# Optimization experiments

Hardware: AMD Instinct MI355X
Metric: run time of the kernel (lower is better)

Reference implementation:

```python
import jax, jax.numpy as jnp
import numpy as np

K_NEIGHBORS = 5
LEAKY_SLOPE = 0.2
NEG_INF = -1e9


def create_knn(x, k):
    # x: [B, N, D] -> binary adjacency [B, N, N], adj[b,i,j]=1 if j is among
    # the k nearest neighbors of i (squared euclidean distance).
    sq = jnp.sum(x * x, axis=-1)                      # [B, N]
    # d2[b,i,j] = |xi|^2 + |xj|^2 - 2 xi.xj
    d2 = sq[:, :, None] + sq[:, None, :] - 2.0 * jnp.einsum('bid,bjd->bij', x, x)
    _, idx = jax.lax.top_k(-d2, k)                    # [B, N, k] nearest (incl. self)
    B, N, _ = x.shape
    b_idx = jnp.arange(B)[:, None, None]
    i_idx = jnp.arange(N)[None, :, None]
    adj = jnp.zeros((B, N, N), dtype=x.dtype).at[b_idx, i_idx, idx].set(1.0)
    return adj


def gat_layer(x, adj, W, a_src, a_dst):
    # Single-head GAT over dense kNN adjacency.
    h = jnp.einsum('bnd,df->bnf', x, W)               # [B, N, F]
    e_src = jnp.einsum('bnf,f->bn', h, a_src)         # [B, N]
    e_dst = jnp.einsum('bnf,f->bn', h, a_dst)         # [B, N]
    e = e_src[:, :, None] + e_dst[:, None, :]         # [B, N, N]
    e = jax.nn.leaky_relu(e, negative_slope=LEAKY_SLOPE)
    e = jnp.where(adj > 0, e, NEG_INF)
    alpha = jax.nn.softmax(e, axis=-1)                # [B, N, N]
    out = jnp.einsum('bij,bjf->bif', alpha, h)        # [B, N, F]
    return jax.nn.elu(out)


def setup_inputs() -> dict:
    key = jax.random.key(0)
    k1, k2, k3, k4 = jax.random.split(key, 4)
    B, N, D = 256, 196, 2048
    F = D // 4
    return {
        'resnet_features': jax.random.normal(k1, (B, N, D), dtype=jnp.float32),
        'W': jax.random.normal(k2, (D, F), dtype=jnp.float32) * (1.0 / np.sqrt(D)),
        'a_src': jax.random.normal(k3, (F,), dtype=jnp.float32) * (1.0 / np.sqrt(F)),
        'a_dst': jax.random.normal(k4, (F,), dtype=jnp.float32) * (1.0 / np.sqrt(F)),
    }


def reference(resnet_features, W, a_src, a_dst):
    adj = create_knn(resnet_features, K_NEIGHBORS)
    return gat_layer(resnet_features, adj, W, a_src, a_dst)
```

## Files before the change

### kernel.cpp

```cpp
#include <hip/hip_runtime.h>

#define B_  256
#define N_  196
#define D_  2048
#define F_  512
#define ROWS (B_*N_)
#define CAND 8
#define PROWS 208
#define PELEMS (PROWS*32)

typedef _Float16 f16x8 __attribute__((ext_vector_type(8)));
typedef _Float16 f16x4 __attribute__((ext_vector_type(4)));
typedef float    f32x4 __attribute__((ext_vector_type(4)));

static __device__ __forceinline__ float wave_reduce_sum(float v) {
#pragma unroll
  for (int off = 32; off > 0; off >>= 1) v += __shfl_xor(v, off);
  return v;
}

static __device__ __forceinline__ double wave_reduce_sum_d(double v) {
#pragma unroll
  for (int off = 32; off > 0; off >>= 1) v += __shfl_xor(v, off);
  return v;
}

static __device__ __forceinline__ float np_chain16(const float* __restrict__ x, int h) {
  int base = (h >> 3) * 128 + (h & 7);
  float t0 = x[base];
  float r = __fmul_rn(t0, t0);
#pragma unroll
  for (int i = 1; i < 16; ++i) {
    float t = x[base + 8 * i];
    r = __fadd_rn(r, __fmul_rn(t, t));
  }
  return r;
}
static __device__ __forceinline__ float np_sq_row(const float* __restrict__ x, int lane) {
  float ra = np_chain16(x, lane);
  float rb = np_chain16(x, lane + 64);
#pragma unroll
  for (int off = 1; off <= 4; off <<= 1) {
    ra = __fadd_rn(ra, __shfl_xor(ra, off));
    rb = __fadd_rn(rb, __shfl_xor(rb, off));
  }
  float lf[16];
#pragma unroll
  for (int L = 0; L < 8; ++L) { lf[L] = __shfl(ra, L * 8); lf[8 + L] = __shfl(rb, L * 8); }
  float b8[8];
#pragma unroll
  for (int t = 0; t < 8; ++t) b8[t] = __fadd_rn(lf[2 * t], lf[2 * t + 1]);
  float c4[4];
#pragma unroll
  for (int t = 0; t < 4; ++t) c4[t] = __fadd_rn(b8[2 * t], b8[2 * t + 1]);
  return __fadd_rn(__fadd_rn(c4[0], c4[1]), __fadd_rn(c4[2], c4[3]));
}

__global__ __launch_bounds__(256) void wtrans_kernel(const float* __restrict__ W,
                                                     _Float16* __restrict__ Wt2) {
  __shared__ float T[64][68];
  int k0 = blockIdx.x * 64;
  int f0 = blockIdx.y * 64;
  int tid = threadIdx.x;
  int c = tid & 63;
  int r4 = tid >> 6;
#pragma unroll
  for (int p = 0; p < 16; ++p) {
    int r = p * 4 + r4;
    T[r][c] = W[(size_t)(k0 + r) * F_ + f0 + c];
  }
  __syncthreads();
#pragma unroll
  for (int p = 0; p < 16; ++p) {
    int fr = p * 4 + r4;
    int kg = k0 + c;
    Wt2[(size_t)(kg >> 5) * F_ * 32 + (size_t)(f0 + fr) * 32 + (kg & 31)] = (_Float16)T[c][fr];
  }
}

__global__ __launch_bounds__(256, 3) void h_gemm(const float* __restrict__ X,
                                                 const _Float16* __restrict__ Wt2,
                                                 float* __restrict__ H) {
  __shared__ _Float16 Al[2][64][40];
  const int mBase = blockIdx.y * 64;
  const int nBase = blockIdx.x * 256;
  const int tid  = threadIdx.x;
  const int lane = tid & 63;
  const int wave = tid >> 6;
  const int fr_row = lane & 15;
  const int fr_k   = (lane >> 4) * 8;
  const int ar = tid >> 2;
  const int ak = (tid & 3) * 8;
  f32x4 acc[4][4] = {};

  const _Float16* Bb = Wt2 + (size_t)(nBase + wave * 64 + fr_row) * 32 + fr_k;
  const size_t PSTRIDE = (size_t)F_ * 32;

  f16x8 bf[4];
#pragma unroll
  for (int n = 0; n < 4; ++n) bf[n] = *(const f16x8*)&Bb[(size_t)n * 512];

  {
    float4 a0 = *(const float4*)&X[(size_t)(mBase + ar) * D_ + ak];
    float4 a1 = *(const float4*)&X[(size_t)(mBase + ar) * D_ + ak + 4];
    f16x8 ah = { (_Float16)a0.x, (_Float16)a0.y, (_Float16)a0.z, (_Float16)a0.w,
                 (_Float16)a1.x, (_Float16)a1.y, (_Float16)a1.z, (_Float16)a1.w };
    *(f16x8*)&Al[0][ar][ak] = ah;
  }
  __syncthreads();

  for (int t = 0; t < 64; ++t) {
    const int cur = t & 1;
    float4 na0, na1; f16x8 nb[4];
    if (t < 63) {
      const int k0 = (t + 1) * 32;
      na0 = *(const float4*)&X[(size_t)(mBase + ar) * D_ + k0 + ak];
      na1 = *(const float4*)&X[(size_t)(mBase + ar) * D_ + k0 + ak + 4];
      const _Float16* bp = Bb + (size_t)(t + 1) * PSTRIDE;
#pragma unroll
      for (int n = 0; n < 4; ++n) nb[n] = *(const f16x8*)&bp[(size_t)n * 512];
    }
    f16x8 af[4];
#pragma unroll
    for (int m = 0; m < 4; ++m) af[m] = *(const f16x8*)&Al[cur][m * 16 + fr_row][fr_k];
#pragma unroll
    for (int m = 0; m < 4; ++m)
#pragma unroll
      for (int n = 0; n < 4; ++n)
        acc[m][n] = __builtin_amdgcn_mfma_f32_16x16x32_f16(af[m], bf[n], acc[m][n], 0, 0, 0);
    if (t < 63) {
      f16x8 ah = { (_Float16)na0.x, (_Float16)na0.y, (_Float16)na0.z, (_Float16)na0.w,
                   (_Float16)na1.x, (_Float16)na1.y, (_Float16)na1.z, (_Float16)na1.w };
      *(f16x8*)&Al[cur ^ 1][ar][ak] = ah;
#pragma unroll
      for (int n = 0; n < 4; ++n) bf[n] = nb[n];
    }
    __syncthreads();
  }

  const int orow0 = mBase + (lane >> 4) * 4;
#pragma unroll
  for (int m = 0; m < 4; ++m) {
#pragma unroll
    for (int n = 0; n < 4; ++n) {
      int col = nBase + wave * 64 + n * 16 + (lane & 15);
#pragma unroll
      for (int i = 0; i < 4; ++i)
        H[(size_t)(orow0 + m * 16 + i) * F_ + col] = acc[m][n][i];
    }
  }
}

__global__ __launch_bounds__(256, 3) void h_gemm_pan(const float* __restrict__ X,
                                                     const _Float16* __restrict__ Wt2,
                                                     float* __restrict__ H,
                                                     _Float16* __restrict__ Xh,
                                                     float* __restrict__ sqg) {
  __shared__ _Float16 Al[2][64][40];
  __shared__ float sqs[64][4];
  const int mBase = blockIdx.y * 64;
  const int nBase = blockIdx.x * 256;
  const bool emit = (blockIdx.x == 0);
  const int tid  = threadIdx.x;
  const int lane = tid & 63;
  const int wave = tid >> 6;
  const int fr_row = lane & 15;
  const int fr_k   = (lane >> 4) * 8;
  const int ar = tid >> 2;
  const int ak = (tid & 3) * 8;
  f32x4 acc[4][4] = {};
  float sqp = 0.f;

  const int grow = mBase + ar;
  const int bb = grow / N_;
  const int rl = grow - bb * N_;
  _Float16* pRow = Xh + (size_t)bb * 64 * PELEMS + (size_t)rl * 32 + ak;

  const _Float16* Bb = Wt2 + (size_t)(nBase + wave * 64 + fr_row) * 32 + fr_k;
  const size_t PSTRIDE = (size_t)F_ * 32;

  f16x8 bf[4];
#pragma unroll
  for (int n = 0; n < 4; ++n) bf[n] = *(const f16x8*)&Bb[(size_t)n * 512];

  {
    float4 a0 = *(const float4*)&X[(size_t)(mBase + ar) * D_ + ak];
    float4 a1 = *(const float4*)&X[(size_t)(mBase + ar) * D_ + ak + 4];
    f16x8 ah = { (_Float16)a0.x, (_Float16)a0.y, (_Float16)a0.z, (_Float16)a0.w,
                 (_Float16)a1.x, (_Float16)a1.y, (_Float16)a1.z, (_Float16)a1.w };
    *(f16x8*)&Al[0][ar][ak] = ah;
    if (emit) {
      sqp += a0.x*a0.x + a0.y*a0.y + a0.z*a0.z + a0.w*a0.w
           + a1.x*a1.x + a1.y*a1.y + a1.z*a1.z + a1.w*a1.w;
      *(f16x8*)pRow = ah;
    }
  }
  __syncthreads();

  for (int t = 0; t < 64; ++t) {
    const int cur = t & 1;
    float4 na0, na1; f16x8 nb[4];
    if (t < 63) {
      const int k0 = (t + 1) * 32;
      na0 = *(const float4*)&X[(size_t)(mBase + ar) * D_ + k0 + ak];
      na1 = *(const float4*)&X[(size_t)(mBase + ar) * D_ + k0 + ak + 4];
      const _Float16* bp = Bb + (size_t)(t + 1) * PSTRIDE;
#pragma unroll
      for (int n = 0; n < 4; ++n) nb[n] = *(const f16x8*)&bp[(size_t)n * 512];
    }
    f16x8 af[4];
#pragma unroll
    for (int m = 0; m < 4; ++m) af[m] = *(const f16x8*)&Al[cur][m * 16 + fr_row][fr_k];
#pragma unroll
    for (int m = 0; m < 4; ++m)
#pragma unroll
      for (int n = 0; n < 4; ++n)
        acc[m][n] = __builtin_amdgcn_mfma_f32_16x16x32_f16(af[m], bf[n], acc[m][n], 0, 0, 0);
    if (t < 63) {
      f16x8 ah = { (_Float16)na0.x, (_Float16)na0.y, (_Float16)na0.z, (_Float16)na0.w,
                   (_Float16)na1.x, (_Float16)na1.y, (_Float16)na1.z, (_Float16)na1.w };
      *(f16x8*)&Al[cur ^ 1][ar][ak] = ah;
      if (emit) {
        sqp += na0.x*na0.x + na0.y*na0.y + na0.z*na0.z + na0.w*na0.w
             + na1.x*na1.x + na1.y*na1.y + na1.z*na1.z + na1.w*na1.w;
        *(f16x8*)(pRow + (size_t)(t + 1) * PELEMS) = ah;
      }
#pragma unroll
      for (int n = 0; n < 4; ++n) bf[n] = nb[n];
    }
    __syncthreads();
  }

  if (emit) sqs[ar][tid & 3] = sqp;
  __syncthreads();
  if (emit && tid < 64)
    sqg[mBase + tid] = sqs[tid][0] + sqs[tid][1] + sqs[tid][2] + sqs[tid][3];

  const int orow0 = mBase + (lane >> 4) * 4;
#pragma unroll
  for (int m = 0; m < 4; ++m) {
#pragma unroll
    for (int n = 0; n < 4; ++n) {
      int col = nBase + wave * 64 + n * 16 + (lane & 15);
#pragma unroll
      for (int i = 0; i < 4; ++i)
        H[(size_t)(orow0 + m * 16 + i) * F_ + col] = acc[m][n][i];
    }
  }
}

__global__ __launch_bounds__(256) void e_kernel(const float* __restrict__ H,
                                                const float* __restrict__ as,
                                                const float* __restrict__ ad,
                                                float* __restrict__ es,
                                                float* __restrict__ ed) {
  int row  = blockIdx.x * 4 + (threadIdx.x >> 6);
  int lane = threadIdx.x & 63;
  const float* h = H + (size_t)row * F_;
  float s = 0.f, d = 0.f;
#pragma unroll
  for (int p = 0; p < 2; ++p) {
    int col = p * 256 + lane * 4;
    float4 hv = *(const float4*)&h[col];
    float4 av = *(const float4*)&as[col];
    float4 dv = *(const float4*)&ad[col];
    s += hv.x * av.x + hv.y * av.y + hv.z * av.z + hv.w * av.w;
    d += hv.x * dv.x + hv.y * dv.y + hv.z * dv.z + hv.w * dv.w;
  }
  s = wave_reduce_sum(s);
  d = wave_reduce_sum(d);
  if (lane == 0) { es[row] = s; ed[row] = d; }
}

__global__ __launch_bounds__(256, 3) void knn_screen(const float* __restrict__ X,
                                                     int* __restrict__ cand8,
                                                     float* __restrict__ gapw) {
  __shared__ _Float16 T[2][256][40];
  __shared__ float sqA[256];

  const int bi  = blockIdx.x;
  const int xcd = bi & 7;
  const int kk  = bi >> 3;
  const int b   = ((kk >> 2) << 3) | xcd;
  const int i0  = (kk & 3) * 64;

  const int tid  = threadIdx.x;
  const int lane = tid & 63;
  const int wave = tid >> 6;
  const float* Xb = X + (size_t)b * N_ * D_;
  const int fr_row = lane & 15;
  const int fr_k   = (lane >> 4) * 8;
  const int srow = tid >> 3;
  const int skk  = (tid & 7) * 4;

  f32x4 acc[13] = {};
  float sqp[8] = {};

  {
    float4 v[8];
#pragma unroll
    for (int p = 0; p < 8; ++p) {
      int r = p * 32 + srow;
      v[p] = make_float4(0.f, 0.f, 0.f, 0.f);
      if (r < N_) v[p] = *(const float4*)&Xb[(size_t)r * D_ + skk];
    }
#pragma unroll
    for (int p = 0; p < 8; ++p) {
      int r = p * 32 + srow;
      sqp[p] += v[p].x * v[p].x + v[p].y * v[p].y + v[p].z * v[p].z + v[p].w * v[p].w;
      f16x4 h4 = { (_Float16)v[p].x, (_Float16)v[p].y, (_Float16)v[p].z, (_Float16)v[p].w };
      *(f16x4*)&T[0][r][skk] = h4;
    }
  }
  __syncthreads();

  for (int t = 0; t < 64; ++t) {
    const int cur = t & 1;
    float4 nv[8];
    if (t < 63) {
      const int k0 = (t + 1) * 32;
#pragma unroll
      for (int p = 0; p < 8; ++p) {
        int r = p * 32 + srow;
        nv[p] = make_float4(0.f, 0.f, 0.f, 0.f);
        if (r < N_) nv[p] = *(const float4*)&Xb[(size_t)r * D_ + k0 + skk];
      }
    }
    f16x8 a0 = *(const f16x8*)&T[cur][i0 + wave * 16 + fr_row][fr_k];
#pragma unroll
    for (int n = 0; n < 13; ++n) {
      f16x8 bfr = *(const f16x8*)&T[cur][n * 16 + fr_row][fr_k];
      acc[n] = __builtin_amdgcn_mfma_f32_16x16x32_f16(a0, bfr, acc[n], 0, 0, 0);
    }
    if (t < 63) {
#pragma unroll
      for (int p = 0; p < 8; ++p) {
        int r = p * 32 + srow;
        sqp[p] += nv[p].x * nv[p].x + nv[p].y * nv[p].y + nv[p].z * nv[p].z + nv[p].w * nv[p].w;
        f16x4 h4 = { (_Float16)nv[p].x, (_Float16)nv[p].y, (_Float16)nv[p].z, (_Float16)nv[p].w };
        *(f16x4*)&T[cur ^ 1][r][skk] = h4;
      }
    }
    __syncthreads();
  }

#pragma unroll
  for (int p = 0; p < 8; ++p) {
    float s = sqp[p];
    s += __shfl_xor(s, 1); s += __shfl_xor(s, 2); s += __shfl_xor(s, 4);
    if ((lane & 7) == 0) sqA[p * 32 + srow] = s;
  }
  __syncthreads();

  float sqv[13];
#pragma unroll
  for (int n = 0; n < 13; ++n) sqv[n] = sqA[n * 16 + (lane & 15)];
  const int g = lane >> 4;
#pragma unroll
  for (int i = 0; i < 4; ++i) {
    int row_loc = wave * 16 + g * 4 + i;
    float w13[13];
#pragma unroll
    for (int n = 0; n < 13; ++n) {
      int col = n * 16 + (lane & 15);
      w13[n] = (col < N_) ? (sqv[n] - 2.0f * acc[n][i]) : 1e30f;
    }
    int candv[CAND]; float mscv[CAND];
#pragma unroll
    for (int it = 0; it < CAND; ++it) {
      float mv = w13[0]; int mn = 0;
#pragma unroll
      for (int n = 1; n < 13; ++n)
        if (w13[n] < mv) { mv = w13[n]; mn = n; }
      int mcol = mn * 16 + (lane & 15);
#pragma unroll
      for (int off = 1; off <= 8; off <<= 1) {
        float ov = __shfl_xor(mv, off);
        int   oc = __shfl_xor(mcol, off);
        if (ov < mv || (ov == mv && oc < mcol)) { mv = ov; mcol = oc; }
      }
      mscv[it] = mv; candv[it] = mcol;
      int kn = mcol >> 4;
#pragma unroll
      for (int n = 0; n < 13; ++n)
        if (n == kn && (lane & 15) == (mcol & 15)) w13[n] = 1e30f;
    }
    int ig = i0 + row_loc;
    if ((lane & 15) == 0 && ig < N_) {
      size_t o = ((size_t)b * N_ + ig) * CAND;
#pragma unroll
      for (int c = 0; c < CAND; ++c) cand8[o + c] = candv[c];
      gapw[b * N_ + ig] = mscv[5] - mscv[4];
    }
  }
}

__global__ __launch_bounds__(256) void knn_screen_pan(const _Float16* __restrict__ Xh,
                                                      const float* __restrict__ sqg,
                                                      int* __restrict__ cand8,
                                                      float* __restrict__ gapw) {
  const int bi  = blockIdx.x;
  const int xcd = bi & 7;
  const int kk  = bi >> 3;
  const int b   = ((kk >> 2) << 3) | xcd;
  const int i0  = (kk & 3) * 64;

  const int tid  = threadIdx.x;
  const int lane = tid & 63;
  const int wave = tid >> 6;
  if (i0 + wave * 16 >= N_) return;

  const int fr_row = lane & 15;
  const int fr_k   = (lane >> 4) * 8;

  const _Float16* Pb = Xh + (size_t)b * 64 * PELEMS;
  const int aoff = (i0 + wave * 16 + fr_row) * 32 + fr_k;

  f32x4 acc[13] = {};
#pragma unroll 2
  for (int t = 0; t < 64; ++t) {
    const _Float16* P = Pb + (size_t)t * PELEMS;
    f16x8 a0 = *(const f16x8*)&P[aoff];
#pragma unroll
    for (int n = 0; n < 13; ++n) {
      f16x8 bfr = *(const f16x8*)&P[(n * 16 + fr_row) * 32 + fr_k];
      acc[n] = __builtin_amdgcn_mfma_f32_16x16x32_f16(a0, bfr, acc[n], 0, 0, 0);
    }
  }

  float sqv[13];
#pragma unroll
  for (int n = 0; n < 13; ++n) {
    int col = n * 16 + (lane & 15);
    sqv[n] = (col < N_) ? sqg[b * N_ + col] : 0.f;
  }
  const int g = lane >> 4;
#pragma unroll
  for (int i = 0; i < 4; ++i) {
    int row_loc = wave * 16 + g * 4 + i;
    float w13[13];
#pragma unroll
    for (int n = 0; n < 13; ++n) {
      int col = n * 16 + (lane & 15);
      w13[n] = (col < N_) ? (sqv[n] - 2.0f * acc[n][i]) : 1e30f;
    }
    int candv[CAND]; float mscv[CAND];
#pragma unroll
    for (int it = 0; it < CAND; ++it) {
      float mv = w13[0]; int mn = 0;
#pragma unroll
      for (int n = 1; n < 13; ++n)
        if (w13[n] < mv) { mv = w13[n]; mn = n; }
      int mcol = mn * 16 + (lane & 15);
#pragma unroll
      for (int off = 1; off <= 8; off <<= 1) {
        float ov = __shfl_xor(mv, off);
        int   oc = __shfl_xor(mcol, off);
        if (ov < mv || (ov == mv && oc < mcol)) { mv = ov; mcol = oc; }
      }
      mscv[it] = mv; candv[it] = mcol;
      int kn = mcol >> 4;
#pragma unroll
      for (int n = 0; n < 13; ++n)
        if (n == kn && (lane & 15) == (mcol & 15)) w13[n] = 1e30f;
    }
    int ig = i0 + row_loc;
    if ((lane & 15) == 0 && ig < N_) {
      size_t o = ((size_t)b * N_ + ig) * CAND;
#pragma unroll
      for (int c = 0; c < CAND; ++c) cand8[o + c] = candv[c];
      gapw[b * N_ + ig] = mscv[5] - mscv[4];
    }
  }
}

__global__ __launch_bounds__(256) void knn_resolve(const float* __restrict__ X,
                                                   const int* __restrict__ cand8,
                                                   const float* __restrict__ gapw,
                                                   const float* __restrict__ es,
                                                   const float* __restrict__ ed,
                                                   int* __restrict__ idx5,
                                                   float* __restrict__ alpha5) {
  const int gr   = blockIdx.x * 4 + (threadIdx.x >> 6);
  const int lane = threadIdx.x & 63;
  const int b    = gr / N_;
  const int ig   = gr - b * N_;
  const float* Xb = X + (size_t)b * N_ * D_;
  const float* xi = Xb + (size_t)ig * D_;

  int cand[CAND];
#pragma unroll
  for (int c = 0; c < CAND; ++c) cand[c] = cand8[(size_t)gr * CAND + c];
  float gap = gapw[gr];

  int ordj[5];
  if (gap > 0.75f) {
#pragma unroll
    for (int m5 = 0; m5 < 5; ++m5) ordj[m5] = cand[m5];
  } else {
    float4 xr[8];
#pragma unroll
    for (int q = 0; q < 8; ++q) xr[q] = *(const float4*)&xi[q * 256 + lane * 4];
    double s8[CAND];
#pragma unroll
    for (int c = 0; c < CAND; ++c) {
      const float* xj = Xb + (size_t)cand[c] * D_;
      double dsum = 0.0, sqc = 0.0;
#pragma unroll
      for (int q = 0; q < 8; ++q) {
        float4 u = *(const float4*)&xj[q * 256 + lane * 4];
        dsum += (double)xr[q].x * (double)u.x + (double)xr[q].y * (double)u.y
              + (double)xr[q].z * (double)u.z + (double)xr[q].w * (double)u.w;
        sqc  += (double)u.x * (double)u.x + (double)u.y * (double)u.y
              + (double)u.z * (double)u.z + (double)u.w * (double)u.w;
      }
      dsum = wave_reduce_sum_d(dsum);
      sqc  = wave_reduce_sum_d(sqc);
      s8[c] = sqc - 2.0 * dsum;
    }
    int rnk[CAND];
#pragma unroll
    for (int c = 0; c < CAND; ++c) {
      int r = 0;
#pragma unroll
      for (int c2 = 0; c2 < CAND; ++c2)
        if (c2 != c && (s8[c2] < s8[c] || (s8[c2] == s8[c] && cand[c2] < cand[c]))) r++;
      rnk[c] = r;
    }
    double g5 = 0.0, g6 = 0.0;
#pragma unroll
    for (int c = 0; c < CAND; ++c) {
      if (rnk[c] == 4) g5 = s8[c];
      if (rnk[c] == 5) g6 = s8[c];
    }
#pragma unroll
    for (int m5 = 0; m5 < 5; ++m5) {
      int oj = 0;
#pragma unroll
      for (int c = 0; c < CAND; ++c)
        if (rnk[c] == m5) oj = cand[c];
      ordj[m5] = oj;
    }
    if (!(g6 - g5 > 4e-3)) {
      float sqi_ex = np_sq_row(xi, lane);
      float sqc_ex[CAND];
#pragma unroll
      for (int c = 0; c < CAND; ++c)
        sqc_ex[c] = np_sq_row(Xb + (size_t)cand[c] * D_, lane);
      int grp8 = (lane >> 2) & 7;
      int l4 = lane & 3;
      int cj = cand[0];
#pragma unroll
      for (int c = 1; c < CAND; ++c)
        if (grp8 == c) cj = cand[c];
      const float* xjr = Xb + (size_t)cj * D_;
      float aacc = 0.f;
      for (int s5 = 0; s5 < 512; ++s5) {
        int d = s5 * 4 + l4;
        aacc = __fadd_rn(aacc, __fmul_rn(xi[d], xjr[d]));
      }
      float d2c[CAND];
#pragma unroll
      for (int c = 0; c < CAND; ++c) {
        float s0 = __shfl(aacc, c * 4 + 0);
        float s1 = __shfl(aacc, c * 4 + 1);
        float s2 = __shfl(aacc, c * 4 + 2);
        float s3 = __shfl(aacc, c * 4 + 3);
        float G  = __fadd_rn(__fadd_rn(s0, s1), __fadd_rn(s2, s3));
        float Sij = __fadd_rn(sqi_ex, sqc_ex[c]);
        d2c[c] = __fsub_rn(Sij, __fadd_rn(G, G));
      }
      int rnk3[CAND];
#pragma unroll
      for (int c = 0; c < CAND; ++c) {
        int r = 0;
#pragma unroll
        for (int c2 = 0; c2 < CAND; ++c2)
          if (c2 != c && (d2c[c2] < d2c[c] || (d2c[c2] == d2c[c] && cand[c2] < cand[c]))) r++;
        rnk3[c] = r;
      }
#pragma unroll
      for (int m5 = 0; m5 < 5; ++m5) {
        int oj = 0;
#pragma unroll
        for (int c = 0; c < CAND; ++c)
          if (rnk3[c] == m5) oj = cand[c];
        ordj[m5] = oj;
      }
    }
  }
  float ei = es[gr];
  float ev[5];
#pragma unroll
  for (int m5 = 0; m5 < 5; ++m5) {
    float e = ei + ed[b * N_ + ordj[m5]];
    ev[m5] = e > 0.f ? e : 0.2f * e;
  }
  float mx = fmaxf(fmaxf(fmaxf(ev[0], ev[1]), fmaxf(ev[2], ev[3])), ev[4]);
  float p0 = expf(ev[0] - mx), p1 = expf(ev[1] - mx), p2 = expf(ev[2] - mx),
        p3 = expf(ev[3] - mx), p4 = expf(ev[4] - mx);
  float inv = 1.0f / (p0 + p1 + p2 + p3 + p4);
  if (lane == 0) {
    size_t o = (size_t)gr * 5;
    idx5[o + 0] = ordj[0]; alpha5[o + 0] = p0 * inv;
    idx5[o + 1] = ordj[1]; alpha5[o + 1] = p1 * inv;
    idx5[o + 2] = ordj[2]; alpha5[o + 2] = p2 * inv;
    idx5[o + 3] = ordj[3]; alpha5[o + 3] = p3 * inv;
    idx5[o + 4] = ordj[4]; alpha5[o + 4] = p4 * inv;
  }
}

__global__ __launch_bounds__(128) void agg_kernel(const float* __restrict__ H,
                                                  const int* __restrict__ idx5,
                                                  const float* __restrict__ alpha5,
                                                  float* __restrict__ out) {
  int row = blockIdx.x;
  int b = row / N_;
  int t = threadIdx.x;
  size_t base5 = (size_t)row * 5;
  const float* Hb = H + (size_t)b * N_ * F_;
  float ax = 0.f, ay = 0.f, az = 0.f, aw = 0.f;
#pragma unroll
  for (int c = 0; c < 5; ++c) {
    int j   = idx5[base5 + c];
    float a = alpha5[base5 + c];
    float4 hv = *(const float4*)&Hb[(size_t)j * F_ + t * 4];
    ax += a * hv.x; ay += a * hv.y; az += a * hv.z; aw += a * hv.w;
  }
  float4 o;
  o.x = ax > 0.f ? ax : expf(ax) - 1.f;
  o.y = ay > 0.f ? ay : expf(ay) - 1.f;
  o.z = az > 0.f ? az : expf(az) - 1.f;
  o.w = aw > 0.f ? aw : expf(aw) - 1.f;
  *(float4*)&out[(size_t)row * F_ + t * 4] = o;
}

extern "C" void kernel_launch(void* const* d_in, const int* in_sizes, int n_in,
                              void* d_out, int out_size, void* d_ws, size_t ws_size,
                              hipStream_t stream) {
  const float* X    = (const float*)d_in[0];
  const float* W    = (const float*)d_in[1];
  const float* Asrc = (const float*)d_in[2];
  const float* Adst = (const float*)d_in[3];
  float* out = (float*)d_out;

  const size_t OFF_WT  = 0;
  const size_t OFF_ES  = OFF_WT + 2097152;
  const size_t OFF_ED  = OFF_ES + 200704;
  const size_t OFF_IDX = OFF_ED + 200704;
  const size_t OFF_ALP = OFF_IDX + 1003520;
  const size_t OFF_C8  = OFF_ALP + 1003520;
  const size_t OFF_GAP = OFF_C8 + 1605632;
  const size_t OFF_SQG = OFF_GAP + 200704;
  const size_t OFF_H   = OFF_SQG + 200704;
  const size_t OFF_XH  = OFF_H + (size_t)ROWS * F_ * 4;
  const size_t XH_BYTES = (size_t)B_ * 64 * PELEMS * 2;
  const size_t NEED_A  = OFF_XH;
  const size_t NEED_B  = OFF_XH + XH_BYTES;
  if (ws_size < NEED_A) return;

  char* ws = (char*)d_ws;
  _Float16* Wt2 = (_Float16*)(ws + OFF_WT);
  float* es     = (float*)(ws + OFF_ES);
  float* ed     = (float*)(ws + OFF_ED);
  int*   idx5   = (int*)  (ws + OFF_IDX);
  float* alpha5 = (float*)(ws + OFF_ALP);
  int*   cand8  = (int*)  (ws + OFF_C8);
  float* gapw   = (float*)(ws + OFF_GAP);
  float* sqg    = (float*)(ws + OFF_SQG);
  float* H      = (float*)(ws + OFF_H);
  _Float16* Xh  = (_Float16*)(ws + OFF_XH);

  wtrans_kernel<<<dim3(32, 8), 256, 0, stream>>>(W, Wt2);
  if (ws_size >= NEED_B) {
    h_gemm_pan<<<dim3(2, 784), 256, 0, stream>>>(X, Wt2, H, Xh, sqg);
    e_kernel<<<ROWS / 4, 256, 0, stream>>>(H, Asrc, Adst, es, ed);
    knn_screen_pan<<<1024, 256, 0, stream>>>(Xh, sqg, cand8, gapw);
  } else {
    h_gemm<<<dim3(2, 784), 256, 0, stream>>>(X, Wt2, H);
    e_kernel<<<ROWS / 4, 256, 0, stream>>>(H, Asrc, Adst, es, ed);
    knn_screen<<<1024, 256, 0, stream>>>(X, cand8, gapw);
  }
  knn_resolve<<<ROWS / 4, 256, 0, stream>>>(X, cand8, gapw, es, ed, idx5, alpha5);
  agg_kernel<<<ROWS, 128, 0, stream>>>(H, idx5, alpha5, out);
}
```

Before: 696.1 us.

## Widen h_gemm_pan block to cover all 512 output columns per row tile

Each block now has 8 waves and computes the full F=512 width for its 64-row tile, instead of splitting columns across two blocks. X is read from global memory and converted to fp16 once per row instead of twice, and every block emits the fp16 panel and squared norms. The norm reduction now uses shuffles instead of shared memory. The trade-off is larger blocks, fewer of them (784), and lower occupancy per block.

```diff
diff --git a/kernel.cpp b/kernel.cpp
--- a/kernel.cpp
+++ b/kernel.cpp
@@ -151,23 +151,20 @@
   }
 }
 
-__global__ __launch_bounds__(256, 3) void h_gemm_pan(const float* __restrict__ X,
+__global__ __launch_bounds__(512, 2) void h_gemm_pan(const float* __restrict__ X,
                                                      const _Float16* __restrict__ Wt2,
                                                      float* __restrict__ H,
                                                      _Float16* __restrict__ Xh,
                                                      float* __restrict__ sqg) {
   __shared__ _Float16 Al[2][64][40];
-  __shared__ float sqs[64][4];
-  const int mBase = blockIdx.y * 64;
-  const int nBase = blockIdx.x * 256;
-  const bool emit = (blockIdx.x == 0);
+  const int mBase = blockIdx.x * 64;
   const int tid  = threadIdx.x;
   const int lane = tid & 63;
   const int wave = tid >> 6;
   const int fr_row = lane & 15;
   const int fr_k   = (lane >> 4) * 8;
-  const int ar = tid >> 2;
-  const int ak = (tid & 3) * 8;
+  const int ar = tid >> 3;
+  const int ak = (tid & 7) * 4;
   f32x4 acc[4][4] = {};
   float sqp = 0.f;
 
@@ -176,7 +173,7 @@
   const int rl = grow - bb * N_;
   _Float16* pRow = Xh + (size_t)bb * 64 * PELEMS + (size_t)rl * 32 + ak;
 
-  const _Float16* Bb = Wt2 + (size_t)(nBase + wave * 64 + fr_row) * 32 + fr_k;
+  const _Float16* Bb = Wt2 + (size_t)(wave * 64 + fr_row) * 32 + fr_k;
   const size_t PSTRIDE = (size_t)F_ * 32;
 
   f16x8 bf[4];
@@ -184,26 +181,20 @@
   for (int n = 0; n < 4; ++n) bf[n] = *(const f16x8*)&Bb[(size_t)n * 512];
 
   {
-    float4 a0 = *(const float4*)&X[(size_t)(mBase + ar) * D_ + ak];
-    float4 a1 = *(const float4*)&X[(size_t)(mBase + ar) * D_ + ak + 4];
-    f16x8 ah = { (_Float16)a0.x, (_Float16)a0.y, (_Float16)a0.z, (_Float16)a0.w,
-                 (_Float16)a1.x, (_Float16)a1.y, (_Float16)a1.z, (_Float16)a1.w };
-    *(f16x8*)&Al[0][ar][ak] = ah;
-    if (emit) {
-      sqp += a0.x*a0.x + a0.y*a0.y + a0.z*a0.z + a0.w*a0.w
-           + a1.x*a1.x + a1.y*a1.y + a1.z*a1.z + a1.w*a1.w;
-      *(f16x8*)pRow = ah;
-    }
+    float4 a0 = *(const float4*)&X[(size_t)grow * D_ + ak];
+    f16x4 ah = { (_Float16)a0.x, (_Float16)a0.y, (_Float16)a0.z, (_Float16)a0.w };
+    *(f16x4*)&Al[0][ar][ak] = ah;
+    sqp += a0.x * a0.x + a0.y * a0.y + a0.z * a0.z + a0.w * a0.w;
+    *(f16x4*)pRow = ah;
   }
   __syncthreads();
 
   for (int t = 0; t < 64; ++t) {
     const int cur = t & 1;
-    float4 na0, na1; f16x8 nb[4];
+    float4 na; f16x8 nb[4];
     if (t < 63) {
       const int k0 = (t + 1) * 32;
-      na0 = *(const float4*)&X[(size_t)(mBase + ar) * D_ + k0 + ak];
-      na1 = *(const float4*)&X[(size_t)(mBase + ar) * D_ + k0 + ak + 4];
+      na = *(const float4*)&X[(size_t)grow * D_ + k0 + ak];
       const _Float16* bp = Bb + (size_t)(t + 1) * PSTRIDE;
 #pragma unroll
       for (int n = 0; n < 4; ++n) nb[n] = *(const f16x8*)&bp[(size_t)n * 512];
@@ -217,31 +208,28 @@
       for (int n = 0; n < 4; ++n)
         acc[m][n] = __builtin_amdgcn_mfma_f32_16x16x32_f16(af[m], bf[n], acc[m][n], 0, 0, 0);
     if (t < 63) {
-      f16x8 ah = { (_Float16)na0.x, (_Float16)na0.y, (_Float16)na0.z, (_Float16)na0.w,
-                   (_Float16)na1.x, (_Float16)na1.y, (_Float16)na1.z, (_Float16)na1.w };
-      *(f16x8*)&Al[cur ^ 1][ar][ak] = ah;
-      if (emit) {
-        sqp += na0.x*na0.x + na0.y*na0.y + na0.z*na0.z + na0.w*na0.w
-             + na1.x*na1.x + na1.y*na1.y + na1.z*na1.z + na1.w*na1.w;
-        *(f16x8*)(pRow + (size_t)(t + 1) * PELEMS) = ah;
-      }
+      f16x4 nah = { (_Float16)na.x, (_Float16)na.y, (_Float16)na.z, (_Float16)na.w };
+      *(f16x4*)&Al[cur ^ 1][ar][ak] = nah;
+      sqp += na.x * na.x + na.y * na.y + na.z * na.z + na.w * na.w;
+      *(f16x4*)(pRow + (size_t)(t + 1) * PELEMS) = nah;
 #pragma unroll
       for (int n = 0; n < 4; ++n) bf[n] = nb[n];
     }
     __syncthreads();
   }
 
-  if (emit) sqs[ar][tid & 3] = sqp;
-  __syncthreads();
-  if (emit && tid < 64)
-    sqg[mBase + tid] = sqs[tid][0] + sqs[tid][1] + sqs[tid][2] + sqs[tid][3];
+  {
+    float s = sqp;
+    s += __shfl_xor(s, 1); s += __shfl_xor(s, 2); s += __shfl_xor(s, 4);
+    if ((lane & 7) == 0) sqg[grow] = s;
+  }
 
   const int orow0 = mBase + (lane >> 4) * 4;
 #pragma unroll
   for (int m = 0; m < 4; ++m) {
 #pragma unroll
     for (int n = 0; n < 4; ++n) {
-      int col = nBase + wave * 64 + n * 16 + (lane & 15);
+      int col = wave * 64 + n * 16 + (lane & 15);
 #pragma unroll
       for (int i = 0; i < 4; ++i)
         H[(size_t)(orow0 + m * 16 + i) * F_ + col] = acc[m][n][i];
@@ -673,7 +661,7 @@
 
   wtrans_kernel<<<dim3(32, 8), 256, 0, stream>>>(W, Wt2);
   if (ws_size >= NEED_B) {
-    h_gemm_pan<<<dim3(2, 784), 256, 0, stream>>>(X, Wt2, H, Xh, sqg);
+    h_gemm_pan<<<784, 512, 0, stream>>>(X, Wt2, H, Xh, sqg);
     e_kernel<<<ROWS / 4, 256, 0, stream>>>(H, Asrc, Adst, es, ed);
     knn_screen_pan<<<1024, 256, 0, stream>>>(Xh, sqg, cand8, gapw);
   } else {
```

Result: no change. 695.9 us (-0.0%).

## Double the K-step of the H GEMM to 64 and split the fp16 X emission across blocks

Applied to the files above, without the earlier changes.

The H=X·W GEMM main loop now processes 64 K-elements per iteration, with two MFMA passes per LDS stage, so it needs half as many barriers and iterations. The B fragments are now loaded in the same iteration rather than prefetched one step ahead. The fp16 X-panel writes are split between the nBase==0 block and the other block, balancing that store work instead of putting it all on one. Squared norms are reduced with wave shuffles instead of a shared-memory pass. In exchange the LDS tile is larger, and exposed W-load latency may rise because the register prefetch is gone.

```diff
diff --git a/kernel.cpp b/kernel.cpp
--- a/kernel.cpp
+++ b/kernel.cpp
@@ -156,57 +156,69 @@
                                                      float* __restrict__ H,
                                                      _Float16* __restrict__ Xh,
                                                      float* __restrict__ sqg) {
-  __shared__ _Float16 Al[2][64][40];
-  __shared__ float sqs[64][4];
+  __shared__ _Float16 Al[2][64][72];
   const int mBase = blockIdx.y * 64;
   const int nBase = blockIdx.x * 256;
-  const bool emit = (blockIdx.x == 0);
   const int tid  = threadIdx.x;
   const int lane = tid & 63;
   const int wave = tid >> 6;
   const int fr_row = lane & 15;
   const int fr_k   = (lane >> 4) * 8;
   const int ar = tid >> 2;
-  const int ak = (tid & 3) * 8;
+  const int ak = (tid & 3) * 16;
   f32x4 acc[4][4] = {};
   float sqp = 0.f;
 
   const int grow = mBase + ar;
   const int bb = grow / N_;
   const int rl = grow - bb * N_;
-  _Float16* pRow = Xh + (size_t)bb * 64 * PELEMS + (size_t)rl * 32 + ak;
+  _Float16* pRow = Xh + (size_t)bb * 64 * PELEMS + (size_t)rl * 32 + (ak & 31);
+  const int pHalf = (ak >= 32) ? 1 : 0;
+  const bool emitLo = (nBase == 0);
 
   const _Float16* Bb = Wt2 + (size_t)(nBase + wave * 64 + fr_row) * 32 + fr_k;
   const size_t PSTRIDE = (size_t)F_ * 32;
 
-  f16x8 bf[4];
-#pragma unroll
-  for (int n = 0; n < 4; ++n) bf[n] = *(const f16x8*)&Bb[(size_t)n * 512];
-
   {
-    float4 a0 = *(const float4*)&X[(size_t)(mBase + ar) * D_ + ak];
-    float4 a1 = *(const float4*)&X[(size_t)(mBase + ar) * D_ + ak + 4];
-    f16x8 ah = { (_Float16)a0.x, (_Float16)a0.y, (_Float16)a0.z, (_Float16)a0.w,
+    float4 a0 = *(const float4*)&X[(size_t)grow * D_ + ak];
+    float4 a1 = *(const float4*)&X[(size_t)grow * D_ + ak + 4];
+    float4 a2 = *(const float4*)&X[(size_t)grow * D_ + ak + 8];
+    float4 a3 = *(const float4*)&X[(size_t)grow * D_ + ak + 12];
+    sqp += a0.x*a0.x + a0.y*a0.y + a0.z*a0.z + a0.w*a0.w
+         + a1.x*a1.x + a1.y*a1.y + a1.z*a1.z + a1.w*a1.w
+         + a2.x*a2.x + a2.y*a2.y + a2.z*a2.z + a2.w*a2.w
+         + a3.x*a3.x + a3.y*a3.y + a3.z*a3.z + a3.w*a3.w;
+    f16x8 h0 = { (_Float16)a0.x, (_Float16)a0.y, (_Float16)a0.z, (_Float16)a0.w,
                  (_Float16)a1.x, (_Float16)a1.y, (_Float16)a1.z, (_Float16)a1.w };
-    *(f16x8*)&Al[0][ar][ak] = ah;
-    if (emit) {
-      sqp += a0.x*a0.x + a0.y*a0.y + a0.z*a0.z + a0.w*a0.w
-           + a1.x*a1.x + a1.y*a1.y + a1.z*a1.z + a1.w*a1.w;
-      *(f16x8*)pRow = ah;
+    f16x8 h1 = { (_Float16)a2.x, (_Float16)a2.y, (_Float16)a2.z, (_Float16)a2.w,
+                 (_Float16)a3.x, (_Float16)a3.y, (_Float16)a3.z, (_Float16)a3.w };
+    *(f16x8*)&Al[0][ar][ak] = h0;
+    *(f16x8*)&Al[0][ar][ak + 8] = h1;
+    if (emitLo) {
+      _Float16* pd = pRow + (size_t)pHalf * PELEMS;
+      *(f16x8*)pd = h0;
+      *(f16x8*)(pd + 8) = h1;
     }
   }
   __syncthreads();
 
-  for (int t = 0; t < 64; ++t) {
-    const int cur = t & 1;
-    float4 na0, na1; f16x8 nb[4];
-    if (t < 63) {
-      const int k0 = (t + 1) * 32;
-      na0 = *(const float4*)&X[(size_t)(mBase + ar) * D_ + k0 + ak];
-      na1 = *(const float4*)&X[(size_t)(mBase + ar) * D_ + k0 + ak + 4];
-      const _Float16* bp = Bb + (size_t)(t + 1) * PSTRIDE;
-#pragma unroll
-      for (int n = 0; n < 4; ++n) nb[n] = *(const f16x8*)&bp[(size_t)n * 512];
+  for (int s = 0; s < 32; ++s) {
+    const int cur = s & 1;
+    float4 na0, na1, na2, na3;
+    if (s < 31) {
+      const int k0 = (s + 1) * 64;
+      na0 = *(const float4*)&X[(size_t)grow * D_ + k0 + ak];
+      na1 = *(const float4*)&X[(size_t)grow * D_ + k0 + ak + 4];
+      na2 = *(const float4*)&X[(size_t)grow * D_ + k0 + ak + 8];
+      na3 = *(const float4*)&X[(size_t)grow * D_ + k0 + ak + 12];
+    }
+    const _Float16* bpLo = Bb + (size_t)(2 * s) * PSTRIDE;
+    const _Float16* bpHi = bpLo + PSTRIDE;
+    f16x8 bfLo[4], bfHi[4];
+#pragma unroll
+    for (int n = 0; n < 4; ++n) {
+      bfLo[n] = *(const f16x8*)&bpLo[(size_t)n * 512];
+      bfHi[n] = *(const f16x8*)&bpHi[(size_t)n * 512];
     }
     f16x8 af[4];
 #pragma unroll
@@ -215,26 +227,40 @@
     for (int m = 0; m < 4; ++m)
 #pragma unroll
       for (int n = 0; n < 4; ++n)
-        acc[m][n] = __builtin_amdgcn_mfma_f32_16x16x32_f16(af[m], bf[n], acc[m][n], 0, 0, 0);
-    if (t < 63) {
-      f16x8 ah = { (_Float16)na0.x, (_Float16)na0.y, (_Float16)na0.z, (_Float16)na0.w,
+        acc[m][n] = __builtin_amdgcn_mfma_f32_16x16x32_f16(af[m], bfLo[n], acc[m][n], 0, 0, 0);
+#pragma unroll
+    for (int m = 0; m < 4; ++m) af[m] = *(const f16x8*)&Al[cur][m * 16 + fr_row][32 + fr_k];
+#pragma unroll
+    for (int m = 0; m < 4; ++m)
+#pragma unroll
+      for (int n = 0; n < 4; ++n)
+        acc[m][n] = __builtin_amdgcn_mfma_f32_16x16x32_f16(af[m], bfHi[n], acc[m][n], 0, 0, 0);
+    if (s < 31) {
+      sqp += na0.x*na0.x + na0.y*na0.y + na0.z*na0.z + na0.w*na0.w
+           + na1.x*na1.x + na1.y*na1.y + na1.z*na1.z + na1.w*na1.w
+           + na2.x*na2.x + na2.y*na2.y + na2.z*na2.z + na2.w*na2.w
+           + na3.x*na3.x + na3.y*na3.y + na3.z*na3.z + na3.w*na3.w;
+      f16x8 h0 = { (_Float16)na0.x, (_Float16)na0.y, (_Float16)na0.z, (_Float16)na0.w,
                    (_Float16)na1.x, (_Float16)na1.y, (_Float16)na1.z, (_Float16)na1.w };
-      *(f16x8*)&Al[cur ^ 1][ar][ak] = ah;
-      if (emit) {
-        sqp += na0.x*na0.x + na0.y*na0.y + na0.z*na0.z + na0.w*na0.w
-             + na1.x*na1.x + na1.y*na1.y + na1.z*na1.z + na1.w*na1.w;
-        *(f16x8*)(pRow + (size_t)(t + 1) * PELEMS) = ah;
-      }
-#pragma unroll
-      for (int n = 0; n < 4; ++n) bf[n] = nb[n];
+      f16x8 h1 = { (_Float16)na2.x, (_Float16)na2.y, (_Float16)na2.z, (_Float16)na2.w,
+                   (_Float16)na3.x, (_Float16)na3.y, (_Float16)na3.z, (_Float16)na3.w };
+      *(f16x8*)&Al[cur ^ 1][ar][ak] = h0;
+      *(f16x8*)&Al[cur ^ 1][ar][ak + 8] = h1;
+      const int sn = s + 1;
+      if ((emitLo && sn < 16) || (!emitLo && sn >= 16)) {
+        _Float16* pd = pRow + (size_t)(2 * sn + pHalf) * PELEMS;
+        *(f16x8*)pd = h0;
+        *(f16x8*)(pd + 8) = h1;
+      }
     }
     __syncthreads();
   }
 
-  if (emit) sqs[ar][tid & 3] = sqp;
-  __syncthreads();
-  if (emit && tid < 64)
-    sqg[mBase + tid] = sqs[tid][0] + sqs[tid][1] + sqs[tid][2] + sqs[tid][3];
+  {
+    float ssum = sqp;
+    ssum += __shfl_xor(ssum, 1); ssum += __shfl_xor(ssum, 2);
+    if (emitLo && (lane & 3) == 0) sqg[grow] = ssum;
+  }
 
   const int orow0 = mBase + (lane >> 4) * 4;
 #pragma unroll
```

Result: slower. 732.9 us (+5.3%).
